# Optimization experiments

Measured on AMD Instinct MI355X. Metric: run time of the kernel, lower is better.

Reference implementation:

```python
import jax, jax.numpy as jnp
import numpy as np

NUM_PATCHES = 10
SIGMA = 4.0            # size_exp_deadzone
PAD_X = 16             # padding_deadzone_size_x
PAD_Y = 16             # padding_deadzone_size_y
DEADZONE_EXP = True
HARD_CUTOUT = True     # deadzone_hard_cutout == 1
HARD_CUTOUT_SIZE = 4.0


def setup_inputs() -> dict:
    key = jax.random.key(0)
    k1, k2, k3, k4 = jax.random.split(key, 4)
    B, C, H, W = 8, 1, 256, 256
    D, KH, KW = 64, 1, 33
    inp = {
        "input": jax.random.normal(k1, (B, C, H, W), dtype=jnp.float32),
        "dictionary_filter": jax.random.normal(k2, (64, C, 33, 33), dtype=jnp.float32),
        "dictionary": jax.random.normal(k3, (64, C, 33, 33), dtype=jnp.float32),
        "dictionary_prior": jax.random.uniform(k4, (64,), dtype=jnp.float32),
    }
    return inp


def _fourier_convolution(contour, dictionary_filter):
    # contour: [B,C,H,W], dictionary_filter: [D,C,kh,kw] (kh,kw odd)
    B, C, H, W = contour.shape
    D, _, kh, kw = dictionary_filter.shape
    filt = jnp.flip(dictionary_filter, axis=(-2, -1))
    padded = jnp.zeros((D, C, H, W), dtype=contour.dtype).at[:, :, :kh, :kw].set(filt)
    padded = jnp.roll(padded, shift=(-(kh // 2), -(kw // 2)), axis=(-2, -1))
    filt_fft = jnp.fft.rfft2(padded)                 # [D,C,H,W//2+1]
    contour_fft = jnp.fft.rfft2(contour)             # [B,C,H,W//2+1]
    # [B,D,C,H,W] -> sum over channel C -> [B,D,H,W]
    conv = jnp.fft.irfft2(contour_fft[:, None] * filt_fft[None], s=(H, W)).sum(axis=2)
    return conv


def reference(input, dictionary_filter, dictionary, dictionary_prior):
    B, C, H, W = input.shape
    dt = input.dtype
    conv = _fourier_convolution(input, dictionary_filter)  # [B,D,H,W]

    use_map = jnp.ones((B, H, W), dtype=dt)
    if PAD_X > 0:
        use_map = use_map.at[:, :PAD_X, :].set(0.0).at[:, -PAD_X:, :].set(0.0)
    if PAD_Y > 0:
        use_map = use_map.at[:, :, :PAD_Y].set(0.0).at[:, :, -PAD_Y:].set(0.0)

    xs = jnp.arange(H, dtype=dt)
    ys = jnp.arange(W, dtype=dt)
    batch_idx = jnp.arange(B)

    def step(use_map, _):
        # search tensor: conv * use_map * prior  -> [B,D,H,W]
        search = conv * use_map[:, None] * dictionary_prior[None, :, None, None]
        flat = search.reshape(B, -1)
        idx = jnp.argmax(flat, axis=1)                    # [B]
        ov0 = jnp.max(flat, axis=1)                       # saliency incl. prior
        d = idx // (H * W)
        rem = idx % (H * W)
        px = rem // W
        py = rem % W
        ov1 = conv[batch_idx, d, px, py]                  # raw overlap
        # deadzone centered at (px,py)
        dx = xs[None, :] - px[:, None].astype(dt)         # [B,H]
        dy = ys[None, :] - py[:, None].astype(dt)         # [B,W]
        dist2 = dx[:, :, None] ** 2 + dy[:, None, :] ** 2  # [B,H,W]
        if DEADZONE_EXP:
            tmap = 1.0 - jnp.exp(-dist2 / (2.0 * SIGMA ** 2))
        else:
            tmap = jnp.ones_like(dist2)
        if HARD_CUTOUT:
            tmap = tmap * jnp.where(dist2 <= HARD_CUTOUT_SIZE ** 2, 0.0, 1.0)
        new_use = use_map * tmap
        new_use = new_use / jnp.max(new_use, axis=(1, 2), keepdims=True)
        pos = jnp.stack([d, px, py], axis=1)              # [B,3]
        ov = jnp.stack([ov0, ov1], axis=1)                # [B,2]
        return new_use, (pos, ov)

    _, (pos, ov) = jax.lax.scan(step, use_map, None, length=NUM_PATCHES)
    position_found = jnp.transpose(pos, (1, 0, 2))  # [B, num_patches, 3] int
    overlap_found = jnp.transpose(ov, (1, 0, 2))    # [B, num_patches, 2]
    return position_found, overlap_found
```

## Files before the change

### kernel.cpp

```cpp
#include <hip/hip_runtime.h>

typedef unsigned long long u64;
typedef unsigned int u32;
typedef unsigned short ushort_t;

using f32x16 = __attribute__((ext_vector_type(16))) float;
using f32x4  = __attribute__((ext_vector_type(4))) float;
using short8 = __attribute__((ext_vector_type(8))) short;

#define NB 8
#define NPIX 65536
#define CAND_CAP 65536
#define MARGIN 45.0f

__device__ __forceinline__ u32 fsort(float f){
  u32 u = __float_as_uint(f);
  return (u & 0x80000000u) ? ~u : (u | 0x80000000u);
}
__device__ __forceinline__ float funsort(u32 s){
  u32 u = (s & 0x80000000u) ? (s ^ 0x80000000u) : ~s;
  return __uint_as_float(u);
}
__device__ __forceinline__ u32 rneb(float f){
  u32 x = __float_as_uint(f);
  return (x + 0x7fffu + ((x >> 16) & 1u)) >> 16;
}
__device__ __forceinline__ float bf2f(u32 h){ return __uint_as_float(h << 16); }

__global__ __launch_bounds__(256) void prep_kernel(
    const float* __restrict__ filt, const float* __restrict__ prior,
    ushort_t* __restrict__ afh, ushort_t* __restrict__ acolh,
    float* __restrict__ fcorner, float* __restrict__ priorR,
    u32* __restrict__ ncand, u32* __restrict__ mmax)
{
  int t = blockIdx.x * 256 + threadIdx.x;
  if (t == 0) *ncand = 0u;
  if (t < 8) mmax[t] = 0u;
  for (int i = t; i < 67584; i += 16384){
    int j = i & 7; int fidx = i >> 3; int lane = fidx & 63; int rest = fidx >> 6;
    int dt = rest & 1; int kc = (rest >> 1) & 1; int fy = rest >> 2;
    int d = dt * 32 + (lane & 31);
    int fx = 16 * kc + 8 * (lane >> 5) + j;
    afh[i] = (ushort_t)rneb(filt[d * 1089 + fy * 33 + fx]);
  }
  for (int i = t; i < 2048; i += 16384){
    int j = i & 7; int fidx = i >> 3; int lane = fidx & 63; int rest = fidx >> 6;
    int dt = rest & 1; int kc = rest >> 1;
    int d = dt * 32 + (lane & 31);
    int fy = 16 * kc + 8 * (lane >> 5) + j;
    acolh[i] = (ushort_t)rneb(filt[d * 1089 + fy * 33 + 32]);
  }
  for (int i = t; i < 2048; i += 16384){
    int reg = i & 15; int rest = i >> 4; int lane = rest & 63; int dt = rest >> 6;
    int d = dt * 32 + (reg & 3) + 8 * (reg >> 2) + 4 * (lane >> 5);
    fcorner[i] = filt[d * 1089 + 1088];
    priorR[i] = prior[d];
  }
}

__device__ __forceinline__ u32 funnel(u32 hi, u32 lo, int sh){
  return (u32)((((u64)hi << 32) | (u64)lo) >> sh);
}
template<int J>
__device__ __forceinline__ short8 extractf(uint4 P0, uint4 P1, int sh){
  u32 W[8] = {P0.x, P0.y, P0.z, P0.w, P1.x, P1.y, P1.z, P1.w};
  uint4 t;
  t.x = funnel(W[J + 1], W[J + 0], sh);
  t.y = funnel(W[J + 2], W[J + 1], sh);
  t.z = funnel(W[J + 3], W[J + 2], sh);
  t.w = funnel(W[J + 4], W[J + 3], sh);
  return __builtin_bit_cast(short8, t);
}
__device__ __forceinline__ f32x16 zero16(){
  f32x16 v;
  #pragma unroll
  for (int i = 0; i < 16; ++i) v[i] = 0.f;
  return v;
}

template<int J>
__device__ __forceinline__ void conv_body(
    const char* ldsc, const ushort_t* lds16, int w, int l, int tX,
    const short8* __restrict__ afh8, const short8* __restrict__ acol8,
    const f32x4* __restrict__ fcp, const f32x4* __restrict__ prp,
    u64* __restrict__ pb, int sh)
{
  const int c = l & 31, h = l >> 5;
  const int y0 = w;
  int cob0[2], cob1[2];
  #pragma unroll
  for (int kc = 0; kc < 2; ++kc){
    int yp = (y0 + 8 * c + 16 * kc + 8 * h - 16) & 255;
    int b0 = yp >> 3, b1 = (b0 + 1) & 31;
    cob0[kc] = b0 * 16; cob1[kc] = b1 * 16;
  }
  const int cc = (y0 + 8 * c + 16) & 255;

#define LA(DST, FY)                                                           \
  { _Pragma("unroll")                                                         \
    for (int kc = 0; kc < 2; ++kc)                                            \
      _Pragma("unroll")                                                       \
      for (int dt = 0; dt < 2; ++dt)                                          \
        DST[kc][dt] = afh8[(((FY) * 2 + kc) * 2 + dt) * 64 + l]; }

#define LW(S, ROWI)                                                           \
  { const char* rb_ = ldsc + (ROWI) * 512;                                    \
    s##S##k0p0 = *(const uint4*)(rb_ + cob0[0]);                              \
    s##S##k0p1 = *(const uint4*)(rb_ + cob1[0]);                              \
    s##S##k1p0 = *(const uint4*)(rb_ + cob0[1]);                              \
    s##S##k1p1 = *(const uint4*)(rb_ + cob1[1]); }

#define CPH(SA, SB, ACUR, ANXT, FYP, DOPF)                                    \
  { if (DOPF){ LA(ANXT, FYP) }                                                \
    short8 b0k0 = extractf<J>(s##SA##k0p0, s##SA##k0p1, sh);                  \
    short8 b0k1 = extractf<J>(s##SA##k1p0, s##SA##k1p1, sh);                  \
    short8 b1k0 = extractf<J>(s##SB##k0p0, s##SB##k0p1, sh);                  \
    short8 b1k1 = extractf<J>(s##SB##k1p0, s##SB##k1p1, sh);                  \
    acc[0][0] = __builtin_amdgcn_mfma_f32_32x32x16_bf16(ACUR[0][0], b0k0, acc[0][0], 0, 0, 0); \
    acc[0][0] = __builtin_amdgcn_mfma_f32_32x32x16_bf16(ACUR[1][0], b0k1, acc[0][0], 0, 0, 0); \
    acc[0][1] = __builtin_amdgcn_mfma_f32_32x32x16_bf16(ACUR[0][1], b0k0, acc[0][1], 0, 0, 0); \
    acc[0][1] = __builtin_amdgcn_mfma_f32_32x32x16_bf16(ACUR[1][1], b0k1, acc[0][1], 0, 0, 0); \
    acc[1][0] = __builtin_amdgcn_mfma_f32_32x32x16_bf16(ACUR[0][0], b1k0, acc[1][0], 0, 0, 0); \
    acc[1][0] = __builtin_amdgcn_mfma_f32_32x32x16_bf16(ACUR[1][0], b1k1, acc[1][0], 0, 0, 0); \
    acc[1][1] = __builtin_amdgcn_mfma_f32_32x32x16_bf16(ACUR[0][1], b1k0, acc[1][1], 0, 0, 0); \
    acc[1][1] = __builtin_amdgcn_mfma_f32_32x32x16_bf16(ACUR[1][1], b1k1, acc[1][1], 0, 0, 0); }

  for (int g0 = 0; g0 < 2; ++g0){
    const int r0 = g0 * 2;
    f32x16 acc[2][2];
    #pragma unroll
    for (int nr = 0; nr < 2; ++nr)
      #pragma unroll
      for (int dt = 0; dt < 2; ++dt) acc[nr][dt] = zero16();

    uint4 s0k0p0, s0k0p1, s0k1p0, s0k1p1;
    uint4 s1k0p0, s1k0p1, s1k1p0, s1k1p1;
    short8 aA[2][2], aB[2][2];

    LW(0, r0)
    LW(1, r0 + 1)
    LA(aA, 0)

    #pragma unroll 1
    for (int fy2 = 0; fy2 < 32; fy2 += 2){
      CPH(0, 1, aA, aB, fy2 + 1, true)
      LW(0, r0 + fy2 + 2)
      CPH(1, 0, aB, aA, fy2 + 2, true)
      LW(1, r0 + fy2 + 3)
    }
    CPH(0, 1, aA, aB, 0, false)

    #pragma unroll
    for (int nr = 0; nr < 2; ++nr){
      #pragma unroll
      for (int kc = 0; kc < 2; ++kc){
        int base = (r0 + nr + 16 * kc + 8 * h) * 512 + cc * 2;
        u32 v0 = *(const ushort_t*)(ldsc + base + 0 * 512);
        u32 v1 = *(const ushort_t*)(ldsc + base + 1 * 512);
        u32 v2 = *(const ushort_t*)(ldsc + base + 2 * 512);
        u32 v3 = *(const ushort_t*)(ldsc + base + 3 * 512);
        u32 v4 = *(const ushort_t*)(ldsc + base + 4 * 512);
        u32 v5 = *(const ushort_t*)(ldsc + base + 5 * 512);
        u32 v6 = *(const ushort_t*)(ldsc + base + 6 * 512);
        u32 v7 = *(const ushort_t*)(ldsc + base + 7 * 512);
        uint4 t;
        t.x = v0 | (v1 << 16); t.y = v2 | (v3 << 16);
        t.z = v4 | (v5 << 16); t.w = v6 | (v7 << 16);
        short8 Bc = __builtin_bit_cast(short8, t);
        #pragma unroll
        for (int dt = 0; dt < 2; ++dt)
          acc[nr][dt] = __builtin_amdgcn_mfma_f32_32x32x16_bf16(
              acol8[(kc * 2 + dt) * 64 + l], Bc, acc[nr][dt], 0, 0, 0);
      }
    }

    #pragma unroll
    for (int nr = 0; nr < 2; ++nr){
      float cv = bf2f((u32)lds16[(r0 + nr + 32) * 256 + cc]);
      float bv = -3e38f; int bd = 0;
      #pragma unroll
      for (int dt = 0; dt < 2; ++dt){
        #pragma unroll
        for (int q = 0; q < 4; ++q){
          f32x4 fc4 = fcp[(dt * 64 + l) * 4 + q];
          f32x4 pr4 = prp[(dt * 64 + l) * 4 + q];
          #pragma unroll
          for (int e = 0; e < 4; ++e){
            int reg = q * 4 + e;
            float s = (acc[nr][dt][reg] + fc4[e] * cv) * pr4[e];
            int d = dt * 32 + e + 8 * q + 4 * h;
            if (s > bv || (s == bv && d < bd)){ bv = s; bd = d; }
          }
        }
      }
      int x = tX + r0 + nr;
      int y = y0 + 8 * c;
      u64 key = ((u64)fsort(bv) << 32) | (u64)(63 - bd);
      u64 other = __shfl_xor(key, 32);
      if (other > key) key = other;
      if (h == 0) pb[(x << 8) | y] = key;
    }
  }
#undef CPH
#undef LW
#undef LA
}

__global__ __launch_bounds__(512) void conv_mfma(
    const float* __restrict__ input,
    const ushort_t* __restrict__ afh, const ushort_t* __restrict__ acolh,
    const float* __restrict__ fcorner, const float* __restrict__ priorR,
    u64* __restrict__ packed)
{
  __shared__ ushort_t lds[9216];
  const int bS = blockIdx.x;
  const int b  = blockIdx.y;
  const int tX = bS * 4;
  const int tid = threadIdx.x;

  const float* inb = input + b * NPIX;
  for (int k = tid; k < 1152; k += 512){
    int r = k >> 5, u = k & 31;
    int gx = (tX - 16 + r) & 255;
    const float* src = inb + (gx << 8) + (u << 3);
    float4 v1 = *(const float4*)(src);
    float4 v2 = *(const float4*)(src + 4);
    uint4 t;
    t.x = rneb(v1.x) | (rneb(v1.y) << 16);
    t.y = rneb(v1.z) | (rneb(v1.w) << 16);
    t.z = rneb(v2.x) | (rneb(v2.y) << 16);
    t.w = rneb(v2.z) | (rneb(v2.w) << 16);
    *(uint4*)((char*)lds + r * 512 + u * 16) = t;
  }
  __syncthreads();

  const int w = tid >> 6, l = tid & 63;
  u64* pb = packed + b * NPIX;
  const int sh = 16 * (w & 1);
  const char* ldsc = (const char*)lds;
  const short8* afh8 = (const short8*)afh;
  const short8* acol8 = (const short8*)acolh;
  const f32x4* fcp = (const f32x4*)fcorner;
  const f32x4* prp = (const f32x4*)priorR;

  switch ((w >> 1) & 3){
    case 0: conv_body<0>(ldsc, lds, w, l, tX, afh8, acol8, fcp, prp, pb, sh); break;
    case 1: conv_body<1>(ldsc, lds, w, l, tX, afh8, acol8, fcp, prp, pb, sh); break;
    case 2: conv_body<2>(ldsc, lds, w, l, tX, afh8, acol8, fcp, prp, pb, sh); break;
    default: conv_body<3>(ldsc, lds, w, l, tX, afh8, acol8, fcp, prp, pb, sh); break;
  }
}

__global__ __launch_bounds__(256) void bmax_kernel(const u64* __restrict__ packed,
                                                   u32* __restrict__ mmax){
  const int b = blockIdx.y, blk = blockIdx.x, tid = threadIdx.x;
  const u32* ph = (const u32*)(packed + b * NPIX);
  u32 m = 0;
  for (int k = tid; k < 2048; k += 256) m = max(m, ph[2 * (blk * 2048 + k) + 1]);
  __shared__ u32 red[256];
  red[tid] = m; __syncthreads();
  for (int s = 128; s > 0; s >>= 1){
    if (tid < s) red[tid] = max(red[tid], red[tid + s]);
    __syncthreads();
  }
  if (tid == 0) atomicMax(&mmax[b], red[0]);
}

__global__ __launch_bounds__(256) void collect_kernel(const u64* __restrict__ packed,
    const u32* __restrict__ mmax, u32* __restrict__ ncand, u32* __restrict__ cand){
  const int b = blockIdx.y, blk = blockIdx.x, tid = threadIdx.x;
  float M = funsort(mmax[b]);
  u32 tu = fsort(M - MARGIN);
  const u32* ph = (const u32*)(packed + b * NPIX);
  for (int k = tid; k < 2048; k += 256){
    int p = blk * 2048 + k;
    u32 v = ph[2 * p + 1];
    if (v >= tu){
      u32 slot = atomicAdd(ncand, 1u);
      if (slot < CAND_CAP) cand[slot] = ((u32)b << 16) | (u32)p;
    }
  }
}

__global__ __launch_bounds__(64) void rerank_kernel(
    const float* __restrict__ input, const float* __restrict__ filt,
    const float* __restrict__ prior, const u32* __restrict__ ncand,
    const u32* __restrict__ cand, u64* __restrict__ packed)
{
  const int lane = threadIdx.x;
  int n = (int)min(*ncand, (u32)CAND_CAP);
  const float* fb = filt + lane * 1089;
  float pv = prior[lane];
  for (int i = blockIdx.x; i < n; i += 1024){
    u32 v = cand[i];
    int b = v >> 16, p = v & 0xffff;
    int px = p >> 8, py = p & 255;
    int yc = py - 16;
    float s = 0.f;
    for (int fy = 0; fy < 33; ++fy){
      const float* ir = input + b * NPIX + (((px + fy - 16) & 255) << 8);
      const float* fr = fb + fy * 33;
      for (int fx = 0; fx < 33; ++fx)
        s = fmaf(fr[fx], ir[(yc + fx) & 255], s);
    }
    u64 key = ((u64)fsort(s * pv) << 32) | (u64)(63 - lane);
    #pragma unroll
    for (int off = 32; off; off >>= 1){
      u64 o = __shfl_down(key, off);
      if (o > key) key = o;
    }
    if (lane == 0) packed[b * NPIX + p] = key;
  }
}

__global__ __launch_bounds__(1024) void greedy_kernel(
    const u64* __restrict__ packed, const float* __restrict__ prior,
    float* __restrict__ out)
{
  const int b = blockIdx.x;
  const int tid = threadIdx.x;
  const u64* pb = packed + b * NPIX;
  const u32* ph = (const u32*)pb;

  const int x = tid >> 2;
  const int ybase = (tid & 3) << 6;
  const int pbase = (x << 8) + ybase;

  float s[64];
  const bool rowin = (x >= 16 && x < 240);
  #pragma unroll
  for (int i = 0; i < 64; ++i){
    int y = ybase + i;
    float bvv = funsort(ph[2 * (pbase + i) + 1]);
    s[i] = (rowin && y >= 16 && y < 240) ? bvv : 0.0f;
  }
  float tm = -3e38f; int tp = pbase;
  #pragma unroll
  for (int i = 0; i < 64; ++i){
    if (s[i] > tm){ tm = s[i]; tp = pbase + i; }
  }

  __shared__ u64 warr[16];
  __shared__ int spx, spy;
  if (tid == 0){ spx = -100000; spy = -100000; }
  __syncthreads();

  for (int t = 0; t < 10; ++t){
    const int px = spx, py = spy;
    if (px >= 0){
      int dxr = x - px;
      if (dxr >= -24 && dxr <= 24){
        int lo = py - 24 - ybase;
        int hi = py + 24 - ybase;
        if (lo < 64 && hi >= 0){
          float dx2 = (float)(dxr * dxr);
          tm = -3e38f; tp = pbase;
          #pragma unroll
          for (int i = 0; i < 64; ++i){
            if (i >= lo && i <= hi){
              float dy = (float)(ybase + i - py);
              float d2 = dx2 + dy * dy;
              float tmap = 1.f - __expf(d2 * -0.03125f);
              if (d2 <= 16.f) tmap = 0.f;
              s[i] *= tmap;
            }
            if (s[i] > tm){ tm = s[i]; tp = pbase + i; }
          }
        }
      }
    }
    u64 key = ((u64)fsort(tm) << 32) | (u64)(0xFFFFu ^ (u32)tp);
    #pragma unroll
    for (int off = 32; off; off >>= 1){
      u64 o = __shfl_down(key, off);
      if (o > key) key = o;
    }
    if ((tid & 63) == 0) warr[tid >> 6] = key;
    __syncthreads();
    if (tid < 64){
      u64 k2 = (tid < 16) ? warr[tid] : 0ull;
      #pragma unroll
      for (int off = 8; off; off >>= 1){
        u64 o = __shfl_down(k2, off);
        if (o > k2) k2 = o;
      }
      if (tid == 0){
        int id = 0xFFFF ^ (int)(k2 & 0xFFFFull);
        float v = funsort((u32)(k2 >> 32));
        u64 pk = pb[id];
        int d = 63 - (int)(pk & 63ull);
        float bvv = funsort((u32)(pk >> 32));
        int xx = id >> 8, yy = id & 255;
        out[b * 30 + t * 3 + 0] = (float)d;
        out[b * 30 + t * 3 + 1] = (float)xx;
        out[b * 30 + t * 3 + 2] = (float)yy;
        out[240 + b * 20 + t * 2 + 0] = v;
        out[240 + b * 20 + t * 2 + 1] = bvv / prior[d];
        spx = xx; spy = yy;
      }
    }
    __syncthreads();
  }
}

extern "C" void kernel_launch(void* const* d_in, const int* in_sizes, int n_in,
                              void* d_out, int out_size, void* d_ws, size_t ws_size,
                              hipStream_t stream)
{
  const float* input = (const float*)d_in[0];
  const float* filt  = (const float*)d_in[1];
  const float* prior = (const float*)d_in[3];
  float* out = (float*)d_out;

  char* ws = (char*)d_ws;
  u64*      packed  = (u64*)(ws);
  u32*      ncand   = (u32*)  (ws + 4194304);
  u32*      mmax    = (u32*)  (ws + 4194368);
  ushort_t* afh     = (ushort_t*)(ws + 4194432);
  ushort_t* acolh   = (ushort_t*)(ws + 4329600);
  float*    fcorner = (float*)(ws + 4333696);
  float*    priorR  = (float*)(ws + 4341888);
  u32*      cand    = (u32*)  (ws + 4350080);

  prep_kernel<<<64, 256, 0, stream>>>(filt, prior, afh, acolh, fcorner, priorR, ncand, mmax);
  conv_mfma<<<dim3(64, NB), 512, 0, stream>>>(input, afh, acolh, fcorner, priorR, packed);
  bmax_kernel<<<dim3(32, NB), 256, 0, stream>>>(packed, mmax);
  collect_kernel<<<dim3(32, NB), 256, 0, stream>>>(packed, mmax, ncand, cand);
  rerank_kernel<<<1024, 64, 0, stream>>>(input, filt, prior, ncand, cand, packed);
  greedy_kernel<<<NB, 1024, 0, stream>>>(packed, prior, out);
}
```

Baseline: 226.7 us.

## Fuse per-batch max into conv kernel, widen rerank, prioritize MFMA waves

The per-image maximum is now reduced inside the convolution kernel with a wave shuffle and an atomicMax, so the separate bmax kernel and its re-read of the packed buffer go away. The rerank kernel now runs four candidates per 256-thread block and splits the inner dot product across four accumulators to shorten the FMA dependency chain. s_setprio is raised around the MFMA bursts so those waves get issue priority. The trade-offs are extra atomics and shuffles at the end of the conv kernel, and a different floating-point summation order in rerank.

```diff
diff --git a/kernel.cpp b/kernel.cpp
--- a/kernel.cpp
+++ b/kernel.cpp
@@ -83,7 +83,7 @@
     const char* ldsc, const ushort_t* lds16, int w, int l, int tX,
     const short8* __restrict__ afh8, const short8* __restrict__ acol8,
     const f32x4* __restrict__ fcp, const f32x4* __restrict__ prp,
-    u64* __restrict__ pb, int sh)
+    u64* __restrict__ pb, u32* __restrict__ mx, int sh)
 {
   const int c = l & 31, h = l >> 5;
   const int y0 = w;
@@ -95,6 +95,7 @@
     cob0[kc] = b0 * 16; cob1[kc] = b1 * 16;
   }
   const int cc = (y0 + 8 * c + 16) & 255;
+  u64 km = 0ull;
 
 #define LA(DST, FY)                                                           \
   { _Pragma("unroll")                                                         \
@@ -116,6 +117,7 @@
     short8 b0k1 = extractf<J>(s##SA##k1p0, s##SA##k1p1, sh);                  \
     short8 b1k0 = extractf<J>(s##SB##k0p0, s##SB##k0p1, sh);                  \
     short8 b1k1 = extractf<J>(s##SB##k1p0, s##SB##k1p1, sh);                  \
+    __builtin_amdgcn_s_setprio(1);                                            \
     acc[0][0] = __builtin_amdgcn_mfma_f32_32x32x16_bf16(ACUR[0][0], b0k0, acc[0][0], 0, 0, 0); \
     acc[0][0] = __builtin_amdgcn_mfma_f32_32x32x16_bf16(ACUR[1][0], b0k1, acc[0][0], 0, 0, 0); \
     acc[0][1] = __builtin_amdgcn_mfma_f32_32x32x16_bf16(ACUR[0][1], b0k0, acc[0][1], 0, 0, 0); \
@@ -123,7 +125,8 @@
     acc[1][0] = __builtin_amdgcn_mfma_f32_32x32x16_bf16(ACUR[0][0], b1k0, acc[1][0], 0, 0, 0); \
     acc[1][0] = __builtin_amdgcn_mfma_f32_32x32x16_bf16(ACUR[1][0], b1k1, acc[1][0], 0, 0, 0); \
     acc[1][1] = __builtin_amdgcn_mfma_f32_32x32x16_bf16(ACUR[0][1], b1k0, acc[1][1], 0, 0, 0); \
-    acc[1][1] = __builtin_amdgcn_mfma_f32_32x32x16_bf16(ACUR[1][1], b1k1, acc[1][1], 0, 0, 0); }
+    acc[1][1] = __builtin_amdgcn_mfma_f32_32x32x16_bf16(ACUR[1][1], b1k1, acc[1][1], 0, 0, 0); \
+    __builtin_amdgcn_s_setprio(0); }
 
   for (int g0 = 0; g0 < 2; ++g0){
     const int r0 = g0 * 2;
@@ -199,8 +202,15 @@
       u64 other = __shfl_xor(key, 32);
       if (other > key) key = other;
       if (h == 0) pb[(x << 8) | y] = key;
-    }
-  }
+      if (key > km) km = key;
+    }
+  }
+  #pragma unroll
+  for (int off = 32; off; off >>= 1){
+    u64 o = __shfl_down(km, off);
+    if (o > km) km = o;
+  }
+  if (l == 0) atomicMax(mx, (u32)(km >> 32));
 #undef CPH
 #undef LW
 #undef LA
@@ -210,7 +220,7 @@
     const float* __restrict__ input,
     const ushort_t* __restrict__ afh, const ushort_t* __restrict__ acolh,
     const float* __restrict__ fcorner, const float* __restrict__ priorR,
-    u64* __restrict__ packed)
+    u64* __restrict__ packed, u32* __restrict__ mmax)
 {
   __shared__ ushort_t lds[9216];
   const int bS = blockIdx.x;
@@ -236,6 +246,7 @@
 
   const int w = tid >> 6, l = tid & 63;
   u64* pb = packed + b * NPIX;
+  u32* mx = mmax + b;
   const int sh = 16 * (w & 1);
   const char* ldsc = (const char*)lds;
   const short8* afh8 = (const short8*)afh;
@@ -244,26 +255,11 @@
   const f32x4* prp = (const f32x4*)priorR;
 
   switch ((w >> 1) & 3){
-    case 0: conv_body<0>(ldsc, lds, w, l, tX, afh8, acol8, fcp, prp, pb, sh); break;
-    case 1: conv_body<1>(ldsc, lds, w, l, tX, afh8, acol8, fcp, prp, pb, sh); break;
-    case 2: conv_body<2>(ldsc, lds, w, l, tX, afh8, acol8, fcp, prp, pb, sh); break;
-    default: conv_body<3>(ldsc, lds, w, l, tX, afh8, acol8, fcp, prp, pb, sh); break;
-  }
-}
-
-__global__ __launch_bounds__(256) void bmax_kernel(const u64* __restrict__ packed,
-                                                   u32* __restrict__ mmax){
-  const int b = blockIdx.y, blk = blockIdx.x, tid = threadIdx.x;
-  const u32* ph = (const u32*)(packed + b * NPIX);
-  u32 m = 0;
-  for (int k = tid; k < 2048; k += 256) m = max(m, ph[2 * (blk * 2048 + k) + 1]);
-  __shared__ u32 red[256];
-  red[tid] = m; __syncthreads();
-  for (int s = 128; s > 0; s >>= 1){
-    if (tid < s) red[tid] = max(red[tid], red[tid + s]);
-    __syncthreads();
-  }
-  if (tid == 0) atomicMax(&mmax[b], red[0]);
+    case 0: conv_body<0>(ldsc, lds, w, l, tX, afh8, acol8, fcp, prp, pb, mx, sh); break;
+    case 1: conv_body<1>(ldsc, lds, w, l, tX, afh8, acol8, fcp, prp, pb, mx, sh); break;
+    case 2: conv_body<2>(ldsc, lds, w, l, tX, afh8, acol8, fcp, prp, pb, mx, sh); break;
+    default: conv_body<3>(ldsc, lds, w, l, tX, afh8, acol8, fcp, prp, pb, mx, sh); break;
+  }
 }
 
 __global__ __launch_bounds__(256) void collect_kernel(const u64* __restrict__ packed,
@@ -282,27 +278,35 @@
   }
 }
 
-__global__ __launch_bounds__(64) void rerank_kernel(
+__global__ __launch_bounds__(256) void rerank_kernel(
     const float* __restrict__ input, const float* __restrict__ filt,
     const float* __restrict__ prior, const u32* __restrict__ ncand,
     const u32* __restrict__ cand, u64* __restrict__ packed)
 {
-  const int lane = threadIdx.x;
+  const int lane = threadIdx.x & 63;
+  const int wv = threadIdx.x >> 6;
   int n = (int)min(*ncand, (u32)CAND_CAP);
   const float* fb = filt + lane * 1089;
   float pv = prior[lane];
-  for (int i = blockIdx.x; i < n; i += 1024){
+  for (int i = blockIdx.x * 4 + wv; i < n; i += 4096){
     u32 v = cand[i];
     int b = v >> 16, p = v & 0xffff;
     int px = p >> 8, py = p & 255;
     int yc = py - 16;
-    float s = 0.f;
+    float s0 = 0.f, s1 = 0.f, s2 = 0.f, s3 = 0.f;
     for (int fy = 0; fy < 33; ++fy){
       const float* ir = input + b * NPIX + (((px + fy - 16) & 255) << 8);
       const float* fr = fb + fy * 33;
-      for (int fx = 0; fx < 33; ++fx)
-        s = fmaf(fr[fx], ir[(yc + fx) & 255], s);
-    }
+      #pragma unroll
+      for (int q = 0; q < 8; ++q){
+        s0 = fmaf(fr[4*q+0], ir[(yc + 4*q+0) & 255], s0);
+        s1 = fmaf(fr[4*q+1], ir[(yc + 4*q+1) & 255], s1);
+        s2 = fmaf(fr[4*q+2], ir[(yc + 4*q+2) & 255], s2);
+        s3 = fmaf(fr[4*q+3], ir[(yc + 4*q+3) & 255], s3);
+      }
+      s0 = fmaf(fr[32], ir[(yc + 32) & 255], s0);
+    }
+    float s = (s0 + s2) + (s1 + s3);
     u64 key = ((u64)fsort(s * pv) << 32) | (u64)(63 - lane);
     #pragma unroll
     for (int off = 32; off; off >>= 1){
@@ -423,9 +427,8 @@
   u32*      cand    = (u32*)  (ws + 4350080);
 
   prep_kernel<<<64, 256, 0, stream>>>(filt, prior, afh, acolh, fcorner, priorR, ncand, mmax);
-  conv_mfma<<<dim3(64, NB), 512, 0, stream>>>(input, afh, acolh, fcorner, priorR, packed);
-  bmax_kernel<<<dim3(32, NB), 256, 0, stream>>>(packed, mmax);
+  conv_mfma<<<dim3(64, NB), 512, 0, stream>>>(input, afh, acolh, fcorner, priorR, packed, mmax);
   collect_kernel<<<dim3(32, NB), 256, 0, stream>>>(packed, mmax, ncand, cand);
-  rerank_kernel<<<1024, 64, 0, stream>>>(input, filt, prior, ncand, cand, packed);
+  rerank_kernel<<<1024, 256, 0, stream>>>(input, filt, prior, ncand, cand, packed);
   greedy_kernel<<<NB, 1024, 0, stream>>>(packed, prior, out);
 }
```

After: 278.9 us. 23.0% more time.
